# Kernel tuning notes

Measured on AMD Instinct MI355X. Metric: run time of the kernel, lower is better.

Reference implementation:

```python
import jax, jax.numpy as jnp
import numpy as np

DIM = 128        # per-head dim == model width in this module
Q_HEADS = 16
KV_HEADS = 4
WINDOW = 512
BATCH = 4
SEQ = 2048


def setup_inputs() -> dict:
    key = jax.random.key(0)
    k1, k2, k3 = jax.random.split(key, 3)
    x = jax.random.normal(k1, (BATCH, SEQ, DIM), dtype=jnp.float32)
    # fused qkv weight, stored (in, out) so forward is x @ W_qkv
    W_qkv = jax.random.normal(k2, (DIM, (Q_HEADS + 2 * KV_HEADS) * DIM), dtype=jnp.float32) * (DIM ** -0.5)
    W_proj = jax.random.normal(k3, (Q_HEADS * DIM, DIM), dtype=jnp.float32) * ((Q_HEADS * DIM) ** -0.5)
    return {"x": x, "W_qkv": W_qkv, "W_proj": W_proj}


def _gqa_forward(x, W_qkv, W_proj):
    b, s, d = x.shape
    qkv = x @ W_qkv                                    # [b, s, (Hq+2Hkv)*d]
    qkv = qkv.reshape(b, s, Q_HEADS + 2 * KV_HEADS, d).transpose(0, 2, 1, 3)
    q = qkv[:, :Q_HEADS]                               # [b, Hq, s, d]
    k = qkv[:, Q_HEADS:Q_HEADS + KV_HEADS]             # [b, Hkv, s, d]
    v = qkv[:, Q_HEADS + KV_HEADS:]                    # [b, Hkv, s, d]

    # GQA: repeat kv heads to match q heads
    group = Q_HEADS // KV_HEADS
    k = jnp.repeat(k, group, axis=1)                   # [b, Hq, s, d]
    v = jnp.repeat(v, group, axis=1)

    scale = 1.0 / jnp.sqrt(jnp.float32(d))
    scores = jnp.einsum('bhqd,bhkd->bhqk', q, k) * scale   # [b, Hq, s, s]

    q_idx = jnp.arange(s)[:, None]
    kv_idx = jnp.arange(s)[None, :]
    rel = (q_idx - kv_idx).astype(jnp.float32)         # [s, s]
    # per-head ALiBi slope: exp2(-(h+1)*8/Hq), added (sign matches source)
    h = jnp.arange(Q_HEADS, dtype=jnp.float32)
    slopes = jnp.exp2(-((h + 1.0) * 8.0 / Q_HEADS))    # [Hq]
    scores = scores + slopes[None, :, None, None] * rel[None, None, :, :]

    mask = (q_idx >= kv_idx) & ((q_idx - kv_idx) <= WINDOW)
    scores = jnp.where(mask[None, None], scores, -jnp.inf)
    probs = jax.nn.softmax(scores, axis=-1)

    att = jnp.einsum('bhqk,bhkd->bhqd', probs, v)      # [b, Hq, s, d]
    att = att.transpose(0, 2, 1, 3).reshape(b, s, Q_HEADS * d)
    return att @ W_proj                                # [b, s, d]


def reference(x, W_qkv, W_proj):
    return _gqa_forward(x, W_qkv, W_proj)
```

## Files before the change

### kernel.cpp

```cpp
#include <hip/hip_runtime.h>
#include <math.h>

#define DIM_    128
#define QH_     16
#define KVH_    4
#define WIN_    512
#define BATCH_  4
#define SEQ_    2048
#define QKV_LD  3072
#define ATT_LD  2048

#define NX   (BATCH_*SEQ_*DIM_)
#define NWQ  (DIM_*QKV_LD)
#define NWP  (ATT_LD*DIM_)

typedef __attribute__((ext_vector_type(8))) short short8;
typedef __attribute__((ext_vector_type(4))) float f32x4;
typedef unsigned short u16;
typedef unsigned int u32;

__device__ __forceinline__ u16 f2bf(float f) {
    u32 u = __float_as_uint(f);
    u += 0x7fff + ((u >> 16) & 1);
    return (u16)(u >> 16);
}
__device__ __forceinline__ float bf2f(u16 u) {
    return __uint_as_float(((u32)u) << 16);
}
__device__ __forceinline__ u32 pkbf(float a, float b) {
    u32 r;
    __asm__("v_cvt_pk_bf16_f32 %0, %1, %2" : "=v"(r) : "v"(a), "v"(b));
    return r;
}
#define MFMA16 __builtin_amdgcn_mfma_f32_16x16x32_bf16

#if __has_builtin(__builtin_amdgcn_exp2f)
#define EXP2F __builtin_amdgcn_exp2f
#else
#define EXP2F exp2f
#endif

__device__ __forceinline__ void gload_lds16(const u16* g, u16* l) {
    __builtin_amdgcn_global_load_lds(
        (const __attribute__((address_space(1))) unsigned int*)(const void*)g,
        (__attribute__((address_space(3))) unsigned int*)(void*)l, 16, 0, 0);
}

__global__ __launch_bounds__(256) void prep(
    const float* __restrict__ x, const float* __restrict__ Wqkv,
    const float* __restrict__ Wproj,
    u16* __restrict__ xh, u16* __restrict__ wth, u16* __restrict__ wpth)
{
    if (blockIdx.x < 1024) {
        const size_t t = (size_t)blockIdx.x * 256 + threadIdx.x;
        float4 v = *(const float4*)(x + 4 * t);
        ushort4 o;
        o.x = f2bf(v.x); o.y = f2bf(v.y); o.z = f2bf(v.z); o.w = f2bf(v.w);
        *(ushort4*)(xh + 4 * t) = o;
        return;
    }
    __shared__ float T[32][33];
    int tile = blockIdx.x - 1024;
    const float* src; u16* dst; int K, N;
    if (tile < 384) { src = Wqkv;  dst = wth;  K = 128;  N = 3072; }
    else { tile -= 384; src = Wproj; dst = wpth; K = 2048; N = 128; }
    const int ntile = N >> 5;
    const int k0 = (tile / ntile) << 5, n0 = (tile % ntile) << 5;
    const int tx = threadIdx.x & 31, ty = threadIdx.x >> 5;
    #pragma unroll
    for (int i = 0; i < 4; ++i)
        T[ty + 8 * i][tx] = src[(size_t)(k0 + ty + 8 * i) * N + n0 + tx];
    __syncthreads();
    #pragma unroll
    for (int i = 0; i < 4; ++i)
        dst[(size_t)(n0 + ty + 8 * i) * K + k0 + tx] = f2bf(T[tx][ty + 8 * i]);
}

__global__ __launch_bounds__(256) void gemm1_mfma(
    const u16* __restrict__ xh, const u16* __restrict__ wth,
    u16* __restrict__ qkvb, u16* __restrict__ vg)
{
    __shared__ u16 Ab[32][512];
    __shared__ u16 Bb[16][512];
    const int bn = blockIdx.x * 64;
    const int bm = blockIdx.y * 128;
    const int tid = threadIdx.x;
    const int wv = tid >> 6, lane = tid & 63;
    const int lr = lane & 15, quad = lane >> 4;
    const int lo = lane & 15, hi = lane >> 4;

    #pragma unroll
    for (int i = 0; i < 12; ++i) {
        const int idx = wv * 12 + i;
        if (idx < 32) {
            const int mt = idx >> 2, s = idx & 3;
            gload_lds16(xh + (size_t)(bm + mt * 16 + lo) * DIM_ + s * 32 + hi * 8,
                        &Ab[idx][0]);
        } else {
            const int j = idx - 32, nt = j >> 2, s = j & 3;
            gload_lds16(wth + (size_t)(bn + nt * 16 + lo) * DIM_ + s * 32 + hi * 8,
                        &Bb[j][0]);
        }
    }
    __syncthreads();

    const int wr = wv >> 1, wc = wv & 1;
    f32x4 acc[4][2] = {};
    if (bn < 2560) {
        #pragma unroll
        for (int s = 0; s < 4; ++s) {
            short8 af[4], bf[2];
            #pragma unroll
            for (int mt = 0; mt < 4; ++mt)
                af[mt] = *(const short8*)&Ab[(wr * 4 + mt) * 4 + s][lane * 8];
            #pragma unroll
            for (int nt = 0; nt < 2; ++nt)
                bf[nt] = *(const short8*)&Bb[(wc * 2 + nt) * 4 + s][lane * 8];
            #pragma unroll
            for (int mt = 0; mt < 4; ++mt)
                #pragma unroll
                for (int nt = 0; nt < 2; ++nt)
                    acc[mt][nt] = MFMA16(bf[nt], af[mt], acc[mt][nt], 0, 0, 0);
        }
        #pragma unroll
        for (int mt = 0; mt < 4; ++mt)
            #pragma unroll
            for (int nt = 0; nt < 2; ++nt) {
                uint2 o;
                o.x = pkbf(acc[mt][nt][0], acc[mt][nt][1]);
                o.y = pkbf(acc[mt][nt][2], acc[mt][nt][3]);
                *(uint2*)(qkvb
                    + (size_t)(bm + wr * 64 + mt * 16 + lr) * QKV_LD
                    + bn + wc * 32 + nt * 16 + quad * 4) = o;
            }
    } else {
        #pragma unroll
        for (int s = 0; s < 4; ++s) {
            short8 af[4], bf[2];
            #pragma unroll
            for (int mt = 0; mt < 4; ++mt)
                af[mt] = *(const short8*)&Ab[(wr * 4 + mt) * 4 + s][lane * 8];
            #pragma unroll
            for (int nt = 0; nt < 2; ++nt)
                bf[nt] = *(const short8*)&Bb[(wc * 2 + nt) * 4 + s][lane * 8];
            #pragma unroll
            for (int mt = 0; mt < 4; ++mt)
                #pragma unroll
                for (int nt = 0; nt < 2; ++nt)
                    acc[mt][nt] = MFMA16(af[mt], bf[nt], acc[mt][nt], 0, 0, 0);
        }
        #pragma unroll
        for (int mt = 0; mt < 4; ++mt)
            #pragma unroll
            for (int nt = 0; nt < 2; ++nt) {
                const int ncol = bn + wc * 32 + nt * 16 + lr - 2560;
                const int kvh = ncol >> 7, d = ncol & 127;
                const int m0 = bm + wr * 64 + mt * 16 + quad * 4;
                uint2 o;
                o.x = pkbf(acc[mt][nt][0], acc[mt][nt][1]);
                o.y = pkbf(acc[mt][nt][2], acc[mt][nt][3]);
                *(uint2*)(vg + ((size_t)((m0 >> 11) * KVH_ + kvh) * DIM_ + d)
                            * SEQ_ + (m0 & 2047)) = o;
            }
    }
}

__global__ __launch_bounds__(512) void attn_mfma(
    const u16* __restrict__ qkvb, const u16* __restrict__ vg,
    u16* __restrict__ ah)
{
    const int xcd  = blockIdx.x & 7;
    const int idx  = blockIdx.x >> 3;
    const int pair = xcd + 8 * (idx & 1);
    const int qt   = idx >> 1;
    const int b    = pair >> 2, kvh = pair & 3;
    const int q0 = qt << 5;
    const int tid = threadIdx.x;
    const int wv8 = tid >> 6, lane = tid & 63;
    const int hq = wv8 >> 1, mrow = wv8 & 1;
    const int lr = lane & 15, quad = lane >> 4;
    const int h = kvh * 4 + hq;
    const bool oddq = (quad & 1) != 0;

    __shared__ u16 Kb[3][8][512];
    __shared__ u16 Vb[3][8][512];

    const float scale2 = 0.08838834764831845f * 1.4426950408889634f;
    const float slope2 = exp2f(-0.5f * (float)(h + 1)) * 1.4426950408889634f;
    const int jbase = max(0, q0 - WIN_);
    const int nch = (q0 + 32 - jbase) >> 5;
    const size_t rowb = (size_t)b * SEQ_;
    const u16* kg  = qkvb + rowb * QKV_LD + (QH_ + kvh) * DIM_;
    const u16* vgb = vg + (size_t)(b * KVH_ + kvh) * DIM_ * SEQ_;
    const int lo = lane & 15, hi = lane >> 4;

    short8 qf[4];
    {
        const u16* qp = qkvb + (rowb + q0 + mrow * 16 + lr) * QKV_LD
                        + h * DIM_ + quad * 8;
        #pragma unroll
        for (int s = 0; s < 4; ++s) qf[s] = *(const short8*)(qp + 32 * s);
    }

    float alpha0;
    {
        const int q = q0 + mrow * 16 + lr;
        const int rm = (q < WIN_) ? q : WIN_;
        alpha0 = slope2 * (float)(q - rm);
    }

    f32x4 O[8] = {};
    float rs = 0.f;

    #define STAGE(CH, SLOT) do {                                              \
        const int _jk = jbase + ((CH) << 5);                                  \
        gload_lds16(kg + (size_t)(_jk + (wv8 >> 2) * 16 + lo) * QKV_LD        \
                    + (wv8 & 3) * 32 + hi * 8, &Kb[(SLOT)][wv8][0]);          \
        gload_lds16(vgb + (size_t)(wv8 * 16 + lo) * SEQ_ + _jk + hi * 8,      \
                    &Vb[(SLOT)][wv8][0]);                                     \
    } while (0)

    STAGE(0, 0);
    STAGE(1, 1);

    for (int ch = 0; ch < nch; ++ch) {
        const int jk = jbase + (ch << 5);
        const int slot = ch % 3;
        __asm__ volatile("s_waitcnt vmcnt(2)" ::: "memory");
        __asm__ volatile("s_barrier" ::: "memory");
        { const int cn = (ch + 2 < nch) ? (ch + 2) : (nch - 1);
          STAGE(cn, (ch + 2) % 3); }

        u32 pw[2][2];
        const int qm0 = q0 + mrow * 16;
        #pragma unroll
        for (int nt = 0; nt < 2; ++nt) {
            f32x4 c = {0.f, 0.f, 0.f, 0.f};
            __builtin_amdgcn_s_setprio(1);
            #pragma unroll
            for (int s = 0; s < 4; ++s) {
                short8 kf = *(const short8*)&Kb[slot][nt * 4 + s][lane * 8];
                c = MFMA16(kf, qf[s], c, 0, 0, 0);
            }
            __builtin_amdgcn_s_setprio(0);
            const int jknt = jk + nt * 16;
            const float b0 = fmaf(-slope2, (float)(jknt + quad * 4), alpha0);
            float e0, e1, e2, e3;
            if (qm0 >= jknt + 15 && qm0 + 15 <= jknt + WIN_) {
                e0 = EXP2F(fmaf(c[0], scale2, b0));
                e1 = EXP2F(fmaf(c[1], scale2, b0 - slope2));
                e2 = EXP2F(fmaf(c[2], scale2, b0 - 2.f * slope2));
                e3 = EXP2F(fmaf(c[3], scale2, b0 - 3.f * slope2));
            } else {
                const int q = qm0 + lr, j0q = jknt + quad * 4;
                float ee[4];
                #pragma unroll
                for (int r = 0; r < 4; ++r) {
                    const int rel = q - (j0q + r);
                    const float t = fmaf(c[r], scale2, b0 - (float)r * slope2);
                    ee[r] = ((unsigned)rel <= (unsigned)WIN_) ? EXP2F(t) : 0.f;
                }
                e0 = ee[0]; e1 = ee[1]; e2 = ee[2]; e3 = ee[3];
            }
            rs += (e0 + e1) + (e2 + e3);
            pw[nt][0] = pkbf(e0, e1);
            pw[nt][1] = pkbf(e2, e3);
        }

        short8 pa;
        {
            union { u32 w[4]; short8 s; } P;
            #pragma unroll
            for (int w = 0; w < 2; ++w) {
                auto r = __builtin_amdgcn_permlane32_swap(
                    pw[0][w], pw[1][w], false, false);
                const u32 rx = r[0], ry = r[1];
                const u32 sx = (u32)__shfl_xor((int)rx, 16);
                const u32 sy = (u32)__shfl_xor((int)ry, 16);
                P.w[w]     = oddq ? sy : rx;
                P.w[2 + w] = oddq ? ry : sx;
            }
            pa = P.s;
        }

        __builtin_amdgcn_s_setprio(1);
        #pragma unroll
        for (int nt = 0; nt < 8; ++nt) {
            short8 vf = *(const short8*)&Vb[slot][nt][lane * 8];
            O[nt] = MFMA16(vf, pa, O[nt], 0, 0, 0);
        }
        __builtin_amdgcn_s_setprio(0);
    }
    #undef STAGE

    __asm__ volatile("s_waitcnt vmcnt(0)" ::: "memory");

    rs += __shfl_xor(rs, 16);
    rs += __shfl_xor(rs, 32);

    {
        const float inv = 1.0f / rs;
        u16* dst = ah + (rowb + q0 + mrow * 16 + lr) * (size_t)ATT_LD
                   + h * DIM_;
        #pragma unroll
        for (int nt = 0; nt < 8; ++nt) {
            uint2 o;
            o.x = pkbf(O[nt][0] * inv, O[nt][1] * inv);
            o.y = pkbf(O[nt][2] * inv, O[nt][3] * inv);
            *(uint2*)(dst + nt * 16 + quad * 4) = o;
        }
    }
}

__global__ __launch_bounds__(256) void gemm2_mfma(
    const u16* __restrict__ ah, const u16* __restrict__ wpth,
    float* __restrict__ out)
{
    const int bm = blockIdx.x * 16;
    const int wv = threadIdx.x >> 6, lane = threadIdx.x & 63;
    const int lr = lane & 15, quad = lane >> 4;
    const int cq = wv;

    const u16* arow  = ah + (size_t)(bm + lr) * ATT_LD + quad * 8;
    const u16* w0row = wpth + (size_t)(cq * 32 + lr) * ATT_LD + quad * 8;
    const u16* w1row = w0row + (size_t)16 * ATT_LD;

    f32x4 acc0 = {0.f, 0.f, 0.f, 0.f}, acc1 = {0.f, 0.f, 0.f, 0.f};
    #pragma unroll 8
    for (int k0 = 0; k0 < ATT_LD; k0 += 32) {
        short8 a  = *(const short8*)(arow + k0);
        short8 w0 = *(const short8*)(w0row + k0);
        short8 w1 = *(const short8*)(w1row + k0);
        acc0 = MFMA16(w0, a, acc0, 0, 0, 0);
        acc1 = MFMA16(w1, a, acc1, 0, 0, 0);
    }
    float* orow = out + (size_t)(bm + lr) * DIM_ + cq * 32;
    *(float4*)(orow + quad * 4)      = *(float4*)&acc0;
    *(float4*)(orow + 16 + quad * 4) = *(float4*)&acc1;
}

extern "C" void kernel_launch(void* const* d_in, const int* in_sizes, int n_in,
                              void* d_out, int out_size, void* d_ws, size_t ws_size,
                              hipStream_t stream)
{
    const float* x     = (const float*)d_in[0];
    const float* Wqkv  = (const float*)d_in[1];
    const float* Wproj = (const float*)d_in[2];
    float* out = (float*)d_out;

    u16* xh   = (u16*)d_ws;
    u16* wth  = xh   + (size_t)NX;
    u16* wpth = wth  + (size_t)NWQ;
    u16* qkvb = wpth + (size_t)NWP;
    u16* vg   = qkvb + (size_t)8192 * QKV_LD;
    u16* ahp  = vg   + (size_t)BATCH_ * KVH_ * DIM_ * SEQ_;

    prep<<<1024 + 640, 256, 0, stream>>>(x, Wqkv, Wproj, xh, wth, wpth);

    gemm1_mfma<<<dim3(QKV_LD / 64, 8192 / 128), 256, 0, stream>>>(
        xh, wth, qkvb, vg);

    attn_mfma<<<1024, 512, 0, stream>>>(qkvb, vg, ahp);

    gemm2_mfma<<<8192 / 16, 256, 0, stream>>>(ahp, wpth, out);
}
```

Measured before the change: 201.5 us.

## Keep weight fragments in registers in QKV GEMM and split attention launch

The QKV projection kernel now drops shared memory. Each block holds its 64-column weight slice in registers and loops over 512 rows, loading x fragments straight from global memory with double-buffered register prefetch. This cuts the grid from 3072 to 768 blocks and removes the LDS staging and barrier, but it gives fewer blocks for occupancy and raises register pressure. Attention is also split into two half-grid launches with a q-tile offset, which adds one launch and may change scheduling of the uneven causal work.

Result: no change. 202.2 us (+0.4%).

```diff
diff --git a/kernel.cpp b/kernel.cpp
--- a/kernel.cpp
+++ b/kernel.cpp
@@ -80,99 +80,88 @@
     const u16* __restrict__ xh, const u16* __restrict__ wth,
     u16* __restrict__ qkvb, u16* __restrict__ vg)
 {
-    __shared__ u16 Ab[32][512];
-    __shared__ u16 Bb[16][512];
     const int bn = blockIdx.x * 64;
-    const int bm = blockIdx.y * 128;
-    const int tid = threadIdx.x;
-    const int wv = tid >> 6, lane = tid & 63;
-    const int lr = lane & 15, quad = lane >> 4;
+    const int mc = blockIdx.y * 512;
+    const int wv = threadIdx.x >> 6, lane = threadIdx.x & 63;
     const int lo = lane & 15, hi = lane >> 4;
-
+    const int lr = lo, quad = hi;
+
+    short8 bf[4][4];
     #pragma unroll
-    for (int i = 0; i < 12; ++i) {
-        const int idx = wv * 12 + i;
-        if (idx < 32) {
-            const int mt = idx >> 2, s = idx & 3;
-            gload_lds16(xh + (size_t)(bm + mt * 16 + lo) * DIM_ + s * 32 + hi * 8,
-                        &Ab[idx][0]);
-        } else {
-            const int j = idx - 32, nt = j >> 2, s = j & 3;
-            gload_lds16(wth + (size_t)(bn + nt * 16 + lo) * DIM_ + s * 32 + hi * 8,
-                        &Bb[j][0]);
-        }
-    }
-    __syncthreads();
-
-    const int wr = wv >> 1, wc = wv & 1;
-    f32x4 acc[4][2] = {};
-    if (bn < 2560) {
-        #pragma unroll
-        for (int s = 0; s < 4; ++s) {
-            short8 af[4], bf[2];
-            #pragma unroll
-            for (int mt = 0; mt < 4; ++mt)
-                af[mt] = *(const short8*)&Ab[(wr * 4 + mt) * 4 + s][lane * 8];
-            #pragma unroll
-            for (int nt = 0; nt < 2; ++nt)
-                bf[nt] = *(const short8*)&Bb[(wc * 2 + nt) * 4 + s][lane * 8];
-            #pragma unroll
-            for (int mt = 0; mt < 4; ++mt)
-                #pragma unroll
-                for (int nt = 0; nt < 2; ++nt)
-                    acc[mt][nt] = MFMA16(bf[nt], af[mt], acc[mt][nt], 0, 0, 0);
-        }
-        #pragma unroll
-        for (int mt = 0; mt < 4; ++mt)
-            #pragma unroll
-            for (int nt = 0; nt < 2; ++nt) {
-                uint2 o;
-                o.x = pkbf(acc[mt][nt][0], acc[mt][nt][1]);
-                o.y = pkbf(acc[mt][nt][2], acc[mt][nt][3]);
-                *(uint2*)(qkvb
-                    + (size_t)(bm + wr * 64 + mt * 16 + lr) * QKV_LD
-                    + bn + wc * 32 + nt * 16 + quad * 4) = o;
-            }
-    } else {
-        #pragma unroll
-        for (int s = 0; s < 4; ++s) {
-            short8 af[4], bf[2];
-            #pragma unroll
-            for (int mt = 0; mt < 4; ++mt)
-                af[mt] = *(const short8*)&Ab[(wr * 4 + mt) * 4 + s][lane * 8];
-            #pragma unroll
-            for (int nt = 0; nt < 2; ++nt)
-                bf[nt] = *(const short8*)&Bb[(wc * 2 + nt) * 4 + s][lane * 8];
-            #pragma unroll
-            for (int mt = 0; mt < 4; ++mt)
-                #pragma unroll
-                for (int nt = 0; nt < 2; ++nt)
-                    acc[mt][nt] = MFMA16(af[mt], bf[nt], acc[mt][nt], 0, 0, 0);
-        }
-        #pragma unroll
-        for (int mt = 0; mt < 4; ++mt)
-            #pragma unroll
-            for (int nt = 0; nt < 2; ++nt) {
-                const int ncol = bn + wc * 32 + nt * 16 + lr - 2560;
-                const int kvh = ncol >> 7, d = ncol & 127;
-                const int m0 = bm + wr * 64 + mt * 16 + quad * 4;
-                uint2 o;
-                o.x = pkbf(acc[mt][nt][0], acc[mt][nt][1]);
-                o.y = pkbf(acc[mt][nt][2], acc[mt][nt][3]);
-                *(uint2*)(vg + ((size_t)((m0 >> 11) * KVH_ + kvh) * DIM_ + d)
-                            * SEQ_ + (m0 & 2047)) = o;
-            }
-    }
+    for (int nt = 0; nt < 4; ++nt)
+        #pragma unroll
+        for (int s = 0; s < 4; ++s)
+            bf[nt][s] = *(const short8*)(
+                wth + (size_t)(bn + nt * 16 + lo) * DIM_ + s * 32 + hi * 8);
+
+    const bool qk = (bn < 2560);
+    const u16* aA = xh + (size_t)(mc + wv * 16 + lo) * DIM_ + hi * 8;
+
+#define G1BODY(AF, IT) do {                                                   \
+    f32x4 acc[4] = {};                                                        \
+    if (qk) {                                                                 \
+        _Pragma("unroll")                                                     \
+        for (int s = 0; s < 4; ++s)                                           \
+            _Pragma("unroll")                                                 \
+            for (int nt = 0; nt < 4; ++nt)                                    \
+                acc[nt] = MFMA16(bf[nt][s], AF[s], acc[nt], 0, 0, 0);         \
+        const int row = mc + (IT) * 64 + wv * 16 + lr;                        \
+        u16* dst = qkvb + (size_t)row * QKV_LD + bn + quad * 4;               \
+        _Pragma("unroll")                                                     \
+        for (int nt = 0; nt < 4; ++nt) {                                      \
+            uint2 o;                                                          \
+            o.x = pkbf(acc[nt][0], acc[nt][1]);                               \
+            o.y = pkbf(acc[nt][2], acc[nt][3]);                               \
+            *(uint2*)(dst + nt * 16) = o;                                     \
+        }                                                                     \
+    } else {                                                                  \
+        _Pragma("unroll")                                                     \
+        for (int s = 0; s < 4; ++s)                                           \
+            _Pragma("unroll")                                                 \
+            for (int nt = 0; nt < 4; ++nt)                                    \
+                acc[nt] = MFMA16(AF[s], bf[nt][s], acc[nt], 0, 0, 0);         \
+        const int m0 = mc + (IT) * 64 + wv * 16 + quad * 4;                   \
+        const int bb = m0 >> 11, mseq = m0 & 2047;                            \
+        _Pragma("unroll")                                                     \
+        for (int nt = 0; nt < 4; ++nt) {                                      \
+            const int ncol = bn + nt * 16 + lr - 2560;                        \
+            const int kvh = ncol >> 7, d = ncol & 127;                        \
+            uint2 o;                                                          \
+            o.x = pkbf(acc[nt][0], acc[nt][1]);                               \
+            o.y = pkbf(acc[nt][2], acc[nt][3]);                               \
+            *(uint2*)(vg + ((size_t)(bb * KVH_ + kvh) * DIM_ + d) * SEQ_      \
+                      + mseq) = o;                                            \
+        }                                                                     \
+    }                                                                         \
+} while (0)
+
+    short8 afA[4], afB[4];
+    #pragma unroll
+    for (int s = 0; s < 4; ++s) afA[s] = *(const short8*)(aA + s * 32);
+
+    #pragma unroll 1
+    for (int it = 0; it < 8; it += 2) {
+        const u16* aN = aA + (size_t)(it + 1) * 64 * DIM_;
+        #pragma unroll
+        for (int s = 0; s < 4; ++s) afB[s] = *(const short8*)(aN + s * 32);
+        G1BODY(afA, it);
+        const int nx = (it + 2 < 8) ? (it + 2) : 7;
+        const u16* aN2 = aA + (size_t)nx * 64 * DIM_;
+        #pragma unroll
+        for (int s = 0; s < 4; ++s) afA[s] = *(const short8*)(aN2 + s * 32);
+        G1BODY(afB, it + 1);
+    }
+#undef G1BODY
 }
 
 __global__ __launch_bounds__(512) void attn_mfma(
     const u16* __restrict__ qkvb, const u16* __restrict__ vg,
-    u16* __restrict__ ah)
+    u16* __restrict__ ah, int qoff)
 {
     const int xcd  = blockIdx.x & 7;
     const int idx  = blockIdx.x >> 3;
     const int pair = xcd + 8 * (idx & 1);
-    const int qt   = idx >> 1;
+    const int qt   = (idx >> 1) + qoff;
     const int b    = pair >> 2, kvh = pair & 3;
     const int q0 = qt << 5;
     const int tid = threadIdx.x;
@@ -357,10 +346,10 @@
 
     prep<<<1024 + 640, 256, 0, stream>>>(x, Wqkv, Wproj, xh, wth, wpth);
 
-    gemm1_mfma<<<dim3(QKV_LD / 64, 8192 / 128), 256, 0, stream>>>(
-        xh, wth, qkvb, vg);
-
-    attn_mfma<<<1024, 512, 0, stream>>>(qkvb, vg, ahp);
+    gemm1_mfma<<<dim3(48, 16), 256, 0, stream>>>(xh, wth, qkvb, vg);
+
+    attn_mfma<<<512, 512, 0, stream>>>(qkvb, vg, ahp, 0);
+    attn_mfma<<<512, 512, 0, stream>>>(qkvb, vg, ahp, 32);
 
     gemm2_mfma<<<8192 / 16, 256, 0, stream>>>(ahp, wpth, out);
 }
```
